# Performance work log

Measured on AMD Instinct MI355X. Metric: run time of the kernel, lower is better.

The kernel has to match this reference:

```python
import jax, jax.numpy as jnp
import numpy as np

# 8 sign-flip operations: all combinations of (+-1, +-1, +-1), shape [8, 3]
OPS = jnp.array([[i, j, k] for i in (-1, 1) for j in (-1, 1) for k in (-1, 1)],
                dtype=jnp.float32)


def setup_inputs() -> dict:
    key = jax.random.key(0)
    k1, k2 = jax.random.split(key)
    B, N = 256, 4096
    X = jax.random.normal(k1, (B, N, 3), dtype=jnp.float32)
    mask = jnp.ones((B, N), dtype=jnp.float32)
    return {"X": X, "mask": mask}


def reference(X, mask):
    # X: [B, N, 3], mask: [B, N]
    m = mask[..., None]                                   # [B, N, 1]
    center = (X * m).sum(axis=1) / m.sum(axis=1)          # [B, 3]
    # torch: X = X - center.unsqueeze(1) * mask  (subtract center only where masked)
    Xc = X - center[:, None, :] * m                       # [B, N, 3]
    # 3x3 covariance per batch element
    C = jnp.einsum('bpi,bpj->bij', Xc, Xc)                # [B, 3, 3]
    # eigh on detached covariance (no grad through eigendecomposition)
    L, V = jnp.linalg.eigh(jax.lax.stop_gradient(C))      # V: [B, 3, 3]
    # F_ops[b,o,i,j] = ops[o,j] * V[b,i,j]  -> [B, 8, 3, 3]
    F_ops = OPS[None, :, None, :] * V[:, None, :, :]
    # h[b,o,p,i] = sum_j F_ops[b,o,j,i] * Xc[b,p,j]
    h = jnp.einsum('boji,bpj->bopi', F_ops, Xc)           # [B, 8, N, 3]
    h = h.reshape(X.shape[0] * 8, X.shape[1], 3)          # [B*8, N, 3]
    return h, jax.lax.stop_gradient(F_ops), center
```

## Files before the change

### kernel.cpp

```cpp
#include <hip/hip_runtime.h>
#include <math.h>

#ifndef USE_NEW_LARTG
#define USE_NEW_LARTG 1
#endif

#define BB 256
#define NN 4096


__device__ __forceinline__ float ssign_(float a, float b) {
  return (b >= 0.0f) ? fabsf(a) : -fabsf(a);
}

__device__ __forceinline__ float slapy2f_(float x, float y) {
#pragma clang fp contract(off)
  float xa = fabsf(x), ya = fabsf(y);
  float w = fmaxf(xa, ya), z = fminf(xa, ya);
  if (z == 0.0f) return w;
  float q = z / w;
  return w * __fsqrt_rn(1.0f + q * q);
}

__device__ __forceinline__ void slartgf_(float f, float g, float& cs, float& sn, float& r) {
#pragma clang fp contract(off)
#if USE_NEW_LARTG
  if (g == 0.0f) { cs = 1.0f; sn = 0.0f; r = f; }
  else if (f == 0.0f) { cs = 0.0f; sn = (g >= 0.0f) ? 1.0f : -1.0f; r = fabsf(g); }
  else {
    float d = __fsqrt_rn(f * f + g * g);
    cs = fabsf(f) / d;
    r = ssign_(d, f);
    sn = g / r;
  }
#else
  if (g == 0.0f) { cs = 1.0f; sn = 0.0f; r = f; }
  else if (f == 0.0f) { cs = 0.0f; sn = 1.0f; r = g; }
  else {
    float rr = __fsqrt_rn(f * f + g * g);
    cs = f / rr; sn = g / rr; r = rr;
    if (fabsf(f) > fabsf(g) && cs < 0.0f) { cs = -cs; sn = -sn; r = -r; }
  }
#endif
}

__device__ __forceinline__ void slaev2f_(float a, float b, float c, float& rt1, float& rt2,
                                         float& cs1, float& sn1) {
#pragma clang fp contract(off)
  float sm = a + c;
  float df = a - c;
  float adf = fabsf(df);
  float tb = b + b;
  float ab = fabsf(tb);
  float acmx, acmn;
  if (fabsf(a) > fabsf(c)) { acmx = a; acmn = c; } else { acmx = c; acmn = a; }
  float rt;
  if (adf > ab)      { float q = ab / adf; rt = adf * __fsqrt_rn(1.0f + q * q); }
  else if (adf < ab) { float q = adf / ab; rt = ab * __fsqrt_rn(1.0f + q * q); }
  else               { rt = ab * __fsqrt_rn(2.0f); }
  int sgn1;
  if (sm < 0.0f)      { rt1 = 0.5f * (sm - rt); sgn1 = -1; rt2 = (acmx / rt1) * acmn - (b / rt1) * b; }
  else if (sm > 0.0f) { rt1 = 0.5f * (sm + rt); sgn1 = 1;  rt2 = (acmx / rt1) * acmn - (b / rt1) * b; }
  else                { rt1 = 0.5f * rt; rt2 = -0.5f * rt; sgn1 = 1; }
  float cs;
  int sgn2;
  if (df >= 0.0f) { cs = df + rt; sgn2 = 1; } else { cs = df - rt; sgn2 = -1; }
  float acs = fabsf(cs);
  if (acs > ab) {
    float ct = -tb / cs;
    sn1 = 1.0f / __fsqrt_rn(1.0f + ct * ct);
    cs1 = ct * sn1;
  } else {
    if (ab == 0.0f) { cs1 = 1.0f; sn1 = 0.0f; }
    else { float tn = -cs / tb; cs1 = 1.0f / __fsqrt_rn(1.0f + tn * tn); sn1 = tn * cs1; }
  }
  if (sgn1 == sgn2) { float tn = cs1; cs1 = -sn1; sn1 = tn; }
}

#define DGET(i)   ((i) == 1 ? d1 : ((i) == 2 ? d2 : d3))
#define DSET(i,v) do { float _t = (v); int _i = (i); \
  d1 = (_i == 1) ? _t : d1; d2 = (_i == 2) ? _t : d2; d3 = (_i == 3) ? _t : d3; } while (0)
#define EGET(i)   ((i) == 1 ? e1 : e2)
#define ESET(i,v) do { float _t = (v); int _i = (i); \
  e1 = (_i == 1) ? _t : e1; e2 = (_i == 2) ? _t : e2; } while (0)
#define WCGET(i)  ((i) == 1 ? wc1 : wc2)
#define WSGET(i)  ((i) == 1 ? ws1 : ws2)
#define WCSET(i,v) do { float _t = (v); int _i = (i); \
  wc1 = (_i == 1) ? _t : wc1; wc2 = (_i == 2) ? _t : wc2; } while (0)
#define WSSET(i,v) do { float _t = (v); int _i = (i); \
  ws1 = (_i == 1) ? _t : ws1; ws2 = (_i == 2) ? _t : ws2; } while (0)
#define ZGETR(rr,j) ((j) == 1 ? z##rr##1 : ((j) == 2 ? z##rr##2 : z##rr##3))
#define ZSETR(rr,j,v) do { float _zv = (v); int _zj = (j); \
  z##rr##1 = (_zj == 1) ? _zv : z##rr##1; \
  z##rr##2 = (_zj == 2) ? _zv : z##rr##2; \
  z##rr##3 = (_zj == 3) ? _zv : z##rr##3; } while (0)
#define ROTR(rr, hi, lo, cc, ss) do { \
  float _zh = ZGETR(rr, (hi)); float _zl = ZGETR(rr, (lo)); \
  float _nh = (cc) * _zh - (ss) * _zl; \
  float _nl = (ss) * _zh + (cc) * _zl; \
  ZSETR(rr, (hi), _nh); ZSETR(rr, (lo), _nl); } while (0)
#define ROTCOLS(hi, lo, cc, ss) do { \
  ROTR(1, hi, lo, cc, ss); ROTR(2, hi, lo, cc, ss); ROTR(3, hi, lo, cc, ss); } while (0)
#define ZSWAPR(rr, i_, k_) do { \
  float _ta = ZGETR(rr, (i_)); float _tb = ZGETR(rr, (k_)); \
  ZSETR(rr, (i_), _tb); ZSETR(rr, (k_), _ta); } while (0)

__device__ __forceinline__ void eigh3_reg(const float C[3][3], float V[3][3]) {
#pragma clang fp contract(off)
  const float eps = 5.9604645e-08f;
  const float eps2 = eps * eps;
  const float safmin = 1.17549435e-38f;
  const int nmaxit = 90;

  float a11 = C[0][0], a21 = C[1][0], a31 = C[2][0];
  float a22 = C[1][1], a32 = C[2][1], a33 = C[2][2];
  float d1, d2, d3, e1, e2, tau1, v3;
  float z11, z12, z13, z21, z22, z23, z31, z32, z33;
  float wc1 = 0.0f, wc2 = 0.0f, ws1 = 0.0f, ws2 = 0.0f;
  int jtot = 0, l1 = 1;
  int m, l, lend, lsv, lendsv, i, j, k, ii;
  float p, g, r, c, s, f, b, rt1, rt2, tst, anorm, cj, sj;

  float xnorm = fabsf(a31);
  if (xnorm == 0.0f) {
    tau1 = 0.0f; v3 = 0.0f;
    d1 = a11; d2 = a22; d3 = a33; e1 = a21; e2 = a32;
  } else {
    float beta = -ssign_(slapy2f_(a21, xnorm), a21);
    tau1 = (beta - a21) / beta;
    v3 = a31 / (a21 - beta);
    e1 = beta;
    float x1 = tau1 * a22 + tau1 * (a32 * v3);
    float x2 = tau1 * a32 + (tau1 * v3) * a33;
    float al = -0.5f * tau1 * (x1 + x2 * v3);
    float w1 = x1 + al;
    float w2 = x2 + al * v3;
    d1 = a11;
    d2 = (a22 - w1) - w1;
    e2 = (a32 - v3 * w1) - w2;
    d3 = (a33 - v3 * w2) - w2 * v3;
  }
  z11 = 1.0f; z12 = 0.0f; z13 = 0.0f;
  z21 = 0.0f; z22 = 1.0f; z23 = 0.0f;
  z31 = 0.0f; z32 = 0.0f; z33 = 1.0f;

L10:
  if (l1 > 3) goto L160;
  if (l1 > 1) ESET(l1 - 1, 0.0f);
  if (l1 <= 2) {
    for (int mm = l1; mm <= 2; ++mm) {
      tst = fabsf(EGET(mm));
      if (tst == 0.0f) { m = mm; goto L30; }
      if (tst <= (__fsqrt_rn(fabsf(DGET(mm))) * __fsqrt_rn(fabsf(DGET(mm + 1)))) * eps) {
        ESET(mm, 0.0f); m = mm; goto L30;
      }
    }
  }
  m = 3;
L30:
  l = l1; lsv = l; lend = m; lendsv = lend; l1 = m + 1;
  if (lend == l) goto L10;
  anorm = 0.0f;
  for (i = l; i <= lend; ++i) anorm = fmaxf(anorm, fabsf(DGET(i)));
  for (i = l; i <= lend - 1; ++i) anorm = fmaxf(anorm, fabsf(EGET(i)));
  if (anorm == 0.0f) goto L10;
  if (fabsf(DGET(lend)) < fabsf(DGET(l))) { lend = lsv; l = lendsv; }

  if (lend > l) {
L40:
    if (l != lend) {
      for (int mm = l; mm <= lend - 1; ++mm) {
        tst = EGET(mm) * EGET(mm);
        if (tst <= (eps2 * fabsf(DGET(mm))) * fabsf(DGET(mm + 1)) + safmin) { m = mm; goto L60; }
      }
    }
    m = lend;
L60:
    if (m < lend) ESET(m, 0.0f);
    p = DGET(l);
    if (m == l) goto L80;
    if (m == l + 1) {
      slaev2f_(DGET(l), EGET(l), DGET(l + 1), rt1, rt2, c, s);
      WCSET(l, c); WSSET(l, s);
      ROTCOLS(l + 1, l, c, s);
      DSET(l, rt1); DSET(l + 1, rt2); ESET(l, 0.0f);
      l = l + 2;
      if (l <= lend) goto L40;
      goto L140;
    }
    if (jtot == nmaxit) goto L140;
    jtot = jtot + 1;
    g = (DGET(l + 1) - p) / (2.0f * EGET(l));
    r = slapy2f_(g, 1.0f);
    g = DGET(m) - p + EGET(l) / (g + ssign_(r, g));
    s = 1.0f; c = 1.0f; p = 0.0f;
    for (i = m - 1; i >= l; --i) {
      f = s * EGET(i); b = c * EGET(i);
      slartgf_(g, f, c, s, r);
      if (i != m - 1) ESET(i + 1, r);
      g = DGET(i + 1) - p;
      r = (DGET(i) - g) * s + 2.0f * c * b;
      p = s * r;
      DSET(i + 1, g + p);
      g = c * r - b;
      WCSET(i, c); WSSET(i, -s);
    }
    for (j = (m - l + 1) - 1; j >= 1; --j) {
      cj = WCGET(l + j - 1); sj = WSGET(l + j - 1);
      ROTCOLS(l + j, l + j - 1, cj, sj);
    }
    DSET(l, DGET(l) - p);
    ESET(l, g);
    goto L40;
L80:
    DSET(l, p);
    l = l + 1;
    if (l <= lend) goto L40;
    goto L140;
  } else {
L90:
    if (l != lend) {
      for (int mm = l; mm >= lend + 1; --mm) {
        tst = EGET(mm - 1) * EGET(mm - 1);
        if (tst <= (eps2 * fabsf(DGET(mm))) * fabsf(DGET(mm - 1)) + safmin) { m = mm; goto L110; }
      }
    }
    m = lend;
L110:
    if (m > lend) ESET(m - 1, 0.0f);
    p = DGET(l);
    if (m == l) goto L130;
    if (m == l - 1) {
      slaev2f_(DGET(l - 1), EGET(l - 1), DGET(l), rt1, rt2, c, s);
      WCSET(m, c); WSSET(m, s);
      ROTCOLS(l, l - 1, c, s);
      DSET(l - 1, rt1); DSET(l, rt2); ESET(l - 1, 0.0f);
      l = l - 2;
      if (l >= lend) goto L90;
      goto L140;
    }
    if (jtot == nmaxit) goto L140;
    jtot = jtot + 1;
    g = (DGET(l - 1) - p) / (2.0f * EGET(l - 1));
    r = slapy2f_(g, 1.0f);
    g = DGET(m) - p + EGET(l - 1) / (g + ssign_(r, g));
    s = 1.0f; c = 1.0f; p = 0.0f;
    for (i = m; i <= l - 1; ++i) {
      f = s * EGET(i); b = c * EGET(i);
      slartgf_(g, f, c, s, r);
      if (i != m) ESET(i - 1, r);
      g = DGET(i) - p;
      r = (DGET(i + 1) - g) * s + 2.0f * c * b;
      p = s * r;
      DSET(i, g + p);
      g = c * r - b;
      WCSET(i, c); WSSET(i, s);
    }
    for (j = 1; j <= (l - m + 1) - 1; ++j) {
      cj = WCGET(m + j - 1); sj = WSGET(m + j - 1);
      ROTCOLS(m + j, m + j - 1, cj, sj);
    }
    DSET(l, DGET(l) - p);
    ESET(l - 1, g);
    goto L90;
L130:
    DSET(l, p);
    l = l - 1;
    if (l >= lend) goto L90;
    goto L140;
  }
L140:
  if (jtot < nmaxit) goto L10;
  goto L190;
L160:
  for (ii = 2; ii <= 3; ++ii) {
    i = ii - 1; k = i; p = DGET(i);
    for (j = ii; j <= 3; ++j) {
      float dj = DGET(j);
      if (dj < p) { k = j; p = dj; }
    }
    if (k != i) {
      DSET(k, DGET(i)); DSET(i, p);
      ZSWAPR(1, i, k); ZSWAPR(2, i, k); ZSWAPR(3, i, k);
    }
  }
L190:
  if (tau1 != 0.0f) {
    float wj, tmp;
    wj = z21 + z31 * v3; tmp = -(tau1 * wj); z21 = z21 + tmp; z31 = z31 + v3 * tmp;
    wj = z22 + z32 * v3; tmp = -(tau1 * wj); z22 = z22 + tmp; z32 = z32 + v3 * tmp;
    wj = z23 + z33 * v3; tmp = -(tau1 * wj); z23 = z23 + tmp; z33 = z33 + v3 * tmp;
  }
  V[0][0] = z11; V[0][1] = z12; V[0][2] = z13;
  V[1][0] = z21; V[1][1] = z22; V[1][2] = z23;
  V[2][0] = z31; V[2][1] = z32; V[2][2] = z33;
}

__global__ __launch_bounds__(1024, 4) void k_fused2(
    const float* __restrict__ X, const float* __restrict__ mask,
    float* __restrict__ out_fops, float* __restrict__ out_center,
    float* __restrict__ h) {
  int b = blockIdx.x;
  int t = threadIdx.x;

  const float4* Xv = reinterpret_cast<const float4*>(X);
  const float4* Mv = reinterpret_cast<const float4*>(mask);

  int fi = b * 3072 + 3 * t;
  float4 v0 = Xv[fi], v1 = Xv[fi + 1], v2 = Xv[fi + 2];
  float4 mm = Mv[b * 1024 + t];
  float px[4] = {v0.x, v0.w, v1.z, v2.y};
  float py[4] = {v0.y, v1.x, v1.w, v2.z};
  float pz[4] = {v0.z, v1.y, v2.x, v2.w};
  float pm[4] = {mm.x, mm.y, mm.z, mm.w};

  double acc[11];
#pragma unroll
  for (int q = 0; q < 11; ++q) acc[q] = 0.0;
#pragma unroll
  for (int q = 0; q < 4; ++q) {
    double x = px[q], y = py[q], zz = pz[q], m = pm[q];
    acc[0] += m;       acc[1] += m * m;
    acc[2] += m * x;   acc[3] += m * y;   acc[4] += m * zz;
    acc[5] += x * x;   acc[6] += x * y;   acc[7] += x * zz;
    acc[8] += y * y;   acc[9] += y * zz;  acc[10] += zz * zz;
  }
#pragma unroll
  for (int off = 32; off > 0; off >>= 1)
#pragma unroll
    for (int q = 0; q < 11; ++q) acc[q] += __shfl_down(acc[q], off, 64);

  __shared__ double sh[16][11];
  int wid = t >> 6, lane = t & 63;
  if (lane == 0)
    for (int q = 0; q < 11; ++q) sh[wid][q] = acc[q];
  __syncthreads();

  __shared__ float svc[12];
  if (t == 0) {
    double r[11];
#pragma unroll
    for (int q = 0; q < 11; ++q) {
      double s = 0.0;
      for (int w = 0; w < 16; ++w) s += sh[w][q];
      r[q] = s;
    }
    double W = r[0], W2 = r[1];
    double ssum[3] = {r[2], r[3], r[4]};
    double M[3][3] = {{r[5], r[6], r[7]}, {r[6], r[8], r[9]}, {r[7], r[9], r[10]}};
    double cc[3] = {ssum[0] / W, ssum[1] / W, ssum[2] / W};
    float Cf[3][3];
#pragma unroll
    for (int i = 0; i < 3; ++i)
#pragma unroll
      for (int j = 0; j < 3; ++j)
        Cf[i][j] = (float)(M[i][j] - (ssum[i] * cc[j] + cc[i] * ssum[j]) + W2 * cc[i] * cc[j]);
    float Vf[3][3];
    eigh3_reg(Cf, Vf);
    float cf[3] = {(float)cc[0], (float)cc[1], (float)cc[2]};
#pragma unroll
    for (int i = 0; i < 3; ++i)
#pragma unroll
      for (int j = 0; j < 3; ++j) svc[i * 3 + j] = Vf[i][j];
    svc[9] = cf[0]; svc[10] = cf[1]; svc[11] = cf[2];
    out_center[b * 3 + 0] = cf[0];
    out_center[b * 3 + 1] = cf[1];
    out_center[b * 3 + 2] = cf[2];
#pragma unroll
    for (int o = 0; o < 8; ++o) {
      float sgn[3] = {(o & 4) ? 1.f : -1.f, (o & 2) ? 1.f : -1.f, (o & 1) ? 1.f : -1.f};
#pragma unroll
      for (int i = 0; i < 3; ++i)
#pragma unroll
        for (int j = 0; j < 3; ++j)
          out_fops[b * 72 + o * 9 + i * 3 + j] = sgn[j] * Vf[i][j];
    }
  }
  __syncthreads();

  float V0 = svc[0], V1 = svc[1], V2 = svc[2];
  float V3 = svc[3], V4 = svc[4], V5 = svc[5];
  float V6 = svc[6], V7 = svc[7], V8 = svc[8];
  float c0 = svc[9], c1 = svc[10], c2 = svc[11];

  float ya[4], yb[4], yc[4];
#pragma unroll
  for (int q = 0; q < 4; ++q) {
    float xcx = px[q] - c0 * pm[q];
    float xcy = py[q] - c1 * pm[q];
    float xcz = pz[q] - c2 * pm[q];
    ya[q] = V0 * xcx + V3 * xcy + V6 * xcz;
    yb[q] = V1 * xcx + V4 * xcy + V7 * xcz;
    yc[q] = V2 * xcx + V5 * xcy + V8 * xcz;
  }

  __shared__ float ylds[12288];
  float4* yv = reinterpret_cast<float4*>(ylds);
  yv[3 * t]     = make_float4(ya[0], yb[0], yc[0], ya[1]);
  yv[3 * t + 1] = make_float4(yb[1], yc[1], ya[2], yb[2]);
  yv[3 * t + 2] = make_float4(yc[2], ya[3], yb[3], yc[3]);
  __syncthreads();

  uint4 r0 = reinterpret_cast<const uint4*>(ylds)[t];
  uint4 r1 = reinterpret_cast<const uint4*>(ylds)[t + 1024];
  uint4 r2 = reinterpret_cast<const uint4*>(ylds)[t + 2048];

  int c0i = t % 3;
  bool ee0 = (c0i == 0), ee1 = (c0i == 1);

  uint4* hv = reinterpret_cast<uint4*>(h);
  int hb = 3072 * (b * 8);
#pragma unroll
  for (int o = 0; o < 8; ++o) {
    unsigned s0 = (o & 4) ? 0u : 0x80000000u;
    unsigned s1 = (o & 2) ? 0u : 0x80000000u;
    unsigned s2 = (o & 1) ? 0u : 0x80000000u;
    unsigned ma = ee0 ? s0 : (ee1 ? s1 : s2);
    unsigned mb = ee0 ? s1 : (ee1 ? s2 : s0);
    unsigned mc = ee0 ? s2 : (ee1 ? s0 : s1);
    int base = hb + 3072 * o;
    hv[base + t]        = make_uint4(r0.x ^ ma, r0.y ^ mb, r0.z ^ mc, r0.w ^ ma);
    hv[base + t + 1024] = make_uint4(r1.x ^ mb, r1.y ^ mc, r1.z ^ ma, r1.w ^ mb);
    hv[base + t + 2048] = make_uint4(r2.x ^ mc, r2.y ^ ma, r2.z ^ mb, r2.w ^ mc);
  }
}

extern "C" void kernel_launch(void* const* d_in, const int* in_sizes, int n_in,
                              void* d_out, int out_size, void* d_ws, size_t ws_size,
                              hipStream_t stream) {
  const float* X = (const float*)d_in[0];
  const float* mask = (const float*)d_in[1];
  float* out = (float*)d_out;
  float* h = out;
  float* fops = out + (size_t)BB * 8 * NN * 3;
  float* center = fops + (size_t)BB * 8 * 9;

  hipLaunchKernelGGL(k_fused2, dim3(BB), dim3(1024), 0, stream,
                     X, mask, fops, center, h);
}
```

Measured before the change: 35.40 us.

## Split each batch across two blocks with redundant statistics reduction

Launches two 512-thread blocks per batch element instead of one 1024-thread block. Each block redundantly reads the whole batch to compute the mean and covariance and the eigendecomposition, then writes only its half of the 8x output. This doubles the block count and halves per-block LDS to improve occupancy and scheduling across CUs. The cost is twice the input reads and twice the serial eigh work per batch. The sign-mask rotation for the second and third uint4 is adjusted for the new 512-element offsets.

```diff
diff --git a/kernel.cpp b/kernel.cpp
--- a/kernel.cpp
+++ b/kernel.cpp
@@ -296,41 +296,50 @@
   V[2][0] = z31; V[2][1] = z32; V[2][2] = z33;
 }
 
-__global__ __launch_bounds__(1024, 4) void k_fused2(
+__global__ __launch_bounds__(512, 4) void k_fused3(
     const float* __restrict__ X, const float* __restrict__ mask,
     float* __restrict__ out_fops, float* __restrict__ out_center,
     float* __restrict__ h) {
-  int b = blockIdx.x;
+  int blk = blockIdx.x;
+  int b = blk & 255;
+  int s = blk >> 8;
   int t = threadIdx.x;
 
   const float4* Xv = reinterpret_cast<const float4*>(X);
   const float4* Mv = reinterpret_cast<const float4*>(mask);
 
-  int fi = b * 3072 + 3 * t;
-  float4 v0 = Xv[fi], v1 = Xv[fi + 1], v2 = Xv[fi + 2];
-  float4 mm = Mv[b * 1024 + t];
-  float px[4] = {v0.x, v0.w, v1.z, v2.y};
-  float py[4] = {v0.y, v1.x, v1.w, v2.z};
-  float pz[4] = {v0.z, v1.y, v2.x, v2.w};
-  float pm[4] = {mm.x, mm.y, mm.z, mm.w};
-
   double acc[11];
 #pragma unroll
   for (int q = 0; q < 11; ++q) acc[q] = 0.0;
-#pragma unroll
-  for (int q = 0; q < 4; ++q) {
-    double x = px[q], y = py[q], zz = pz[q], m = pm[q];
-    acc[0] += m;       acc[1] += m * m;
-    acc[2] += m * x;   acc[3] += m * y;   acc[4] += m * zz;
-    acc[5] += x * x;   acc[6] += x * y;   acc[7] += x * zz;
-    acc[8] += y * y;   acc[9] += y * zz;  acc[10] += zz * zz;
+  float kx[4], ky[4], kz[4], km[4];
+#pragma unroll
+  for (int half = 0; half < 2; ++half) {
+    int fi = b * 3072 + half * 1536 + 3 * t;
+    float4 v0 = Xv[fi], v1 = Xv[fi + 1], v2 = Xv[fi + 2];
+    float4 mm = Mv[b * 1024 + half * 512 + t];
+    float px[4] = {v0.x, v0.w, v1.z, v2.y};
+    float py[4] = {v0.y, v1.x, v1.w, v2.z};
+    float pz[4] = {v0.z, v1.y, v2.x, v2.w};
+    float pm[4] = {mm.x, mm.y, mm.z, mm.w};
+#pragma unroll
+    for (int q = 0; q < 4; ++q) {
+      double x = px[q], y = py[q], zz = pz[q], m = pm[q];
+      acc[0] += m;       acc[1] += m * m;
+      acc[2] += m * x;   acc[3] += m * y;   acc[4] += m * zz;
+      acc[5] += x * x;   acc[6] += x * y;   acc[7] += x * zz;
+      acc[8] += y * y;   acc[9] += y * zz;  acc[10] += zz * zz;
+    }
+    if (half == s) {
+#pragma unroll
+      for (int q = 0; q < 4; ++q) { kx[q] = px[q]; ky[q] = py[q]; kz[q] = pz[q]; km[q] = pm[q]; }
+    }
   }
 #pragma unroll
   for (int off = 32; off > 0; off >>= 1)
 #pragma unroll
     for (int q = 0; q < 11; ++q) acc[q] += __shfl_down(acc[q], off, 64);
 
-  __shared__ double sh[16][11];
+  __shared__ double sh[8][11];
   int wid = t >> 6, lane = t & 63;
   if (lane == 0)
     for (int q = 0; q < 11; ++q) sh[wid][q] = acc[q];
@@ -341,9 +350,9 @@
     double r[11];
 #pragma unroll
     for (int q = 0; q < 11; ++q) {
-      double s = 0.0;
-      for (int w = 0; w < 16; ++w) s += sh[w][q];
-      r[q] = s;
+      double ss = 0.0;
+      for (int w = 0; w < 8; ++w) ss += sh[w][q];
+      r[q] = ss;
     }
     double W = r[0], W2 = r[1];
     double ssum[3] = {r[2], r[3], r[4]};
@@ -363,17 +372,19 @@
 #pragma unroll
       for (int j = 0; j < 3; ++j) svc[i * 3 + j] = Vf[i][j];
     svc[9] = cf[0]; svc[10] = cf[1]; svc[11] = cf[2];
-    out_center[b * 3 + 0] = cf[0];
-    out_center[b * 3 + 1] = cf[1];
-    out_center[b * 3 + 2] = cf[2];
-#pragma unroll
-    for (int o = 0; o < 8; ++o) {
-      float sgn[3] = {(o & 4) ? 1.f : -1.f, (o & 2) ? 1.f : -1.f, (o & 1) ? 1.f : -1.f};
-#pragma unroll
-      for (int i = 0; i < 3; ++i)
-#pragma unroll
-        for (int j = 0; j < 3; ++j)
-          out_fops[b * 72 + o * 9 + i * 3 + j] = sgn[j] * Vf[i][j];
+    if (s == 0) {
+      out_center[b * 3 + 0] = cf[0];
+      out_center[b * 3 + 1] = cf[1];
+      out_center[b * 3 + 2] = cf[2];
+#pragma unroll
+      for (int o = 0; o < 8; ++o) {
+        float sgn[3] = {(o & 4) ? 1.f : -1.f, (o & 2) ? 1.f : -1.f, (o & 1) ? 1.f : -1.f};
+#pragma unroll
+        for (int i = 0; i < 3; ++i)
+#pragma unroll
+          for (int j = 0; j < 3; ++j)
+            out_fops[b * 72 + o * 9 + i * 3 + j] = sgn[j] * Vf[i][j];
+      }
     }
   }
   __syncthreads();
@@ -386,15 +397,15 @@
   float ya[4], yb[4], yc[4];
 #pragma unroll
   for (int q = 0; q < 4; ++q) {
-    float xcx = px[q] - c0 * pm[q];
-    float xcy = py[q] - c1 * pm[q];
-    float xcz = pz[q] - c2 * pm[q];
+    float xcx = kx[q] - c0 * km[q];
+    float xcy = ky[q] - c1 * km[q];
+    float xcz = kz[q] - c2 * km[q];
     ya[q] = V0 * xcx + V3 * xcy + V6 * xcz;
     yb[q] = V1 * xcx + V4 * xcy + V7 * xcz;
     yc[q] = V2 * xcx + V5 * xcy + V8 * xcz;
   }
 
-  __shared__ float ylds[12288];
+  __shared__ float ylds[6144];
   float4* yv = reinterpret_cast<float4*>(ylds);
   yv[3 * t]     = make_float4(ya[0], yb[0], yc[0], ya[1]);
   yv[3 * t + 1] = make_float4(yb[1], yc[1], ya[2], yb[2]);
@@ -402,26 +413,26 @@
   __syncthreads();
 
   uint4 r0 = reinterpret_cast<const uint4*>(ylds)[t];
-  uint4 r1 = reinterpret_cast<const uint4*>(ylds)[t + 1024];
-  uint4 r2 = reinterpret_cast<const uint4*>(ylds)[t + 2048];
+  uint4 r1 = reinterpret_cast<const uint4*>(ylds)[t + 512];
+  uint4 r2 = reinterpret_cast<const uint4*>(ylds)[t + 1024];
 
   int c0i = t % 3;
   bool ee0 = (c0i == 0), ee1 = (c0i == 1);
 
   uint4* hv = reinterpret_cast<uint4*>(h);
-  int hb = 3072 * (b * 8);
+  int hb = 3072 * (b * 8) + 1536 * s;
 #pragma unroll
   for (int o = 0; o < 8; ++o) {
-    unsigned s0 = (o & 4) ? 0u : 0x80000000u;
-    unsigned s1 = (o & 2) ? 0u : 0x80000000u;
-    unsigned s2 = (o & 1) ? 0u : 0x80000000u;
-    unsigned ma = ee0 ? s0 : (ee1 ? s1 : s2);
-    unsigned mb = ee0 ? s1 : (ee1 ? s2 : s0);
-    unsigned mc = ee0 ? s2 : (ee1 ? s0 : s1);
+    unsigned g0 = (o & 4) ? 0u : 0x80000000u;
+    unsigned g1 = (o & 2) ? 0u : 0x80000000u;
+    unsigned g2 = (o & 1) ? 0u : 0x80000000u;
+    unsigned ma = ee0 ? g0 : (ee1 ? g1 : g2);
+    unsigned mb = ee0 ? g1 : (ee1 ? g2 : g0);
+    unsigned mc = ee0 ? g2 : (ee1 ? g0 : g1);
     int base = hb + 3072 * o;
     hv[base + t]        = make_uint4(r0.x ^ ma, r0.y ^ mb, r0.z ^ mc, r0.w ^ ma);
-    hv[base + t + 1024] = make_uint4(r1.x ^ mb, r1.y ^ mc, r1.z ^ ma, r1.w ^ mb);
-    hv[base + t + 2048] = make_uint4(r2.x ^ mc, r2.y ^ ma, r2.z ^ mb, r2.w ^ mc);
+    hv[base + t + 512]  = make_uint4(r1.x ^ mc, r1.y ^ ma, r1.z ^ mb, r1.w ^ mc);
+    hv[base + t + 1024] = make_uint4(r2.x ^ mb, r2.y ^ mc, r2.z ^ ma, r2.w ^ mb);
   }
 }
 
@@ -435,6 +446,6 @@
   float* fops = out + (size_t)BB * 8 * NN * 3;
   float* center = fops + (size_t)BB * 8 * 9;
 
-  hipLaunchKernelGGL(k_fused2, dim3(BB), dim3(1024), 0, stream,
+  hipLaunchKernelGGL(k_fused3, dim3(BB * 2), dim3(512), 0, stream,
                      X, mask, fops, center, h);
 }
```

After: 32.55 us. 8.1% less time.
